# Kernel optimization log

Hardware: AMD Instinct MI355X
Metric: run time of the kernel (lower is better)

Reference implementation:

```python
import jax, jax.numpy as jnp
import numpy as np

B, T, H, S, A, E = 256, 64, 2048, 512, 64, 2048


def setup_inputs() -> dict:
    key = jax.random.key(0)
    ks = jax.random.split(key, 16)
    def w(k, shape, fan_in):
        return (jax.random.normal(k, shape, dtype=jnp.float32) / np.float32(np.sqrt(fan_in)))
    return {
        "prev_hidden": jax.random.normal(ks[0], (B, H), dtype=jnp.float32),
        "prev_state": jax.random.normal(ks[1], (B, S), dtype=jnp.float32),
        "actions": jax.random.normal(ks[2], (B, T, A), dtype=jnp.float32),
        "obs": jax.random.normal(ks[3], (B, T, E), dtype=jnp.float32),
        "prior_noise": jax.random.normal(ks[4], (B, T - 1, S), dtype=jnp.float32),
        "post_noise": jax.random.normal(ks[5], (B, T - 1, S), dtype=jnp.float32),
        # project_state_action: Linear(A+S -> H), stored [in, out]
        "W_sa": w(ks[6], (S + A, H), S + A), "b_sa": jnp.zeros((H,), jnp.float32),
        # GRUCell weights in torch layout [3H, in]
        "W_ih": w(ks[7], (3 * H, H), H), "W_hh": w(ks[8], (3 * H, H), H),
        "b_ih": jnp.zeros((3 * H,), jnp.float32), "b_hh": jnp.zeros((3 * H,), jnp.float32),
        # project_hidden_action: Linear(H+A -> H)
        "W_ha": w(ks[9], (H + A, H), H + A), "b_ha": jnp.zeros((H,), jnp.float32),
        # prior: Linear(H -> 2S)
        "W_prior": w(ks[10], (H, 2 * S), H), "b_prior": jnp.zeros((2 * S,), jnp.float32),
        # project_hidden_obs: Linear(H+E -> H)
        "W_ho": w(ks[11], (H + E, H), H + E), "b_ho": jnp.zeros((H,), jnp.float32),
        # posterior: Linear(H -> 2S)
        "W_post": w(ks[12], (H, 2 * S), H), "b_post": jnp.zeros((2 * S,), jnp.float32),
        "stop": 0,
    }


def reference(prev_hidden, prev_state, actions, obs, prior_noise, post_noise,
              W_sa, b_sa, W_ih, W_hh, b_ih, b_hh, W_ha, b_ha,
              W_prior, b_prior, W_ho, b_ho, W_post, b_post, stop):
    relu = jax.nn.relu

    def gru(x, h):
        gi = x @ W_ih.T + b_ih  # [B, 3H]
        gh = h @ W_hh.T + b_hh
        ir, iz, inn = jnp.split(gi, 3, axis=-1)
        hr, hz, hn = jnp.split(gh, 3, axis=-1)
        r = jax.nn.sigmoid(ir + hr)
        z = jax.nn.sigmoid(iz + hz)
        n = jnp.tanh(inn + r * hn)
        return (1.0 - z) * n + z * h

    def step(carry, xs):
        h, s = carry  # h: [B,H] hidden, s: [B,S] posterior state (obs is given)
        a, o, pn, qn = xs
        sa = relu(jnp.concatenate([s, a], axis=-1) @ W_sa + b_sa)
        h = gru(sa, h)
        ha = relu(jnp.concatenate([h, a], axis=-1) @ W_ha + b_ha)
        pm, plv = jnp.split(ha @ W_prior + b_prior, 2, axis=-1)
        ps = pm + jnp.exp(jax.nn.softplus(plv)) * pn  # prior rsample
        ho = relu(jnp.concatenate([h, o], axis=-1) @ W_ho + b_ho)
        qm, qlv = jnp.split(ho @ W_post + b_post, 2, axis=-1)
        qs = qm + jnp.exp(jax.nn.softplus(qlv)) * qn  # posterior rsample
        return (h, qs), (h, ps, qs, pm, plv, qm, qlv)

    Tm1 = actions.shape[1] - 1
    xs = (jnp.swapaxes(actions[:, :Tm1], 0, 1),
          jnp.swapaxes(obs[:, :Tm1], 0, 1),
          jnp.swapaxes(prior_noise, 0, 1),
          jnp.swapaxes(post_noise, 0, 1))
    _, ys = jax.lax.scan(step, (prev_hidden, prev_state), xs)
    hs, ps, qs, pm, plv, qm, qlv = (jnp.swapaxes(y, 0, 1) for y in ys)
    hiddens = jnp.concatenate([prev_hidden[:, None, :], hs], axis=1)       # [B, T, H]
    prior_states = jnp.concatenate([prev_state[:, None, :], ps], axis=1)   # [B, T, S]
    posterior_states = jnp.concatenate([prev_state[:, None, :], qs], axis=1)
    return (hiddens, prior_states, posterior_states, pm, plv, qm, qlv)
```

## Files before the change

kernel.cpp:

```cpp
#include <hip/hip_runtime.h>


typedef __attribute__((ext_vector_type(8))) short bf16x8;
typedef __attribute__((ext_vector_type(4))) float f32x4;
typedef __attribute__((ext_vector_type(4))) short s16x4;

#define DEVI static __device__ __forceinline__

DEVI float bf2f(short s) { union { float f; unsigned u; } v; v.u = ((unsigned)(unsigned short)s) << 16; return v.f; }
DEVI short f2bf(float f) {
  union { float f; unsigned u; } v; v.f = f;
  unsigned r = v.u + 0x7FFFu + ((v.u >> 16) & 1u);
  return (short)(r >> 16);
}

#define Bsz 256
#define Tsz 64
#define Hsz 2048
#define Ssz 512
#define Asz 64
#define Esz 2048
#define TM1 63

#define PSH (256 * 2048)
#define PSS (256 * 1024)

#define OUT_PS  33554432L
#define OUT_QS  41943040L
#define OUT_PM  50331648L
#define OUT_PLV 58589184L
#define OUT_QM  66846720L
#define OUT_QLV 75104256L

struct GArg {
  const short* A; const short* Bt; const float* bias; const short* Ci;
  float* oF; short* oB;
  int lda, ldb, ldoF, ldoB; long ldci, pstride;
};

template<int HASBIAS, int HASCI, int RELU, int OUTF, int OUTB>
__global__ __launch_bounds__(256) void gemm_bt(GArg g0, GArg g1, int kcK) {
  const int gemm = blockIdx.z & 1, kc = blockIdx.z >> 1;
  const GArg g = gemm ? g1 : g0;
  const short* __restrict__ Ag = g.A + (long)kc * kcK;
  const short* __restrict__ Bg = g.Bt + (long)kc * kcK;
  __shared__ __align__(16) short As[2][128 * 64];
  __shared__ __align__(16) short Bs[2][128 * 64];
  const int tid = threadIdx.x;
  const int w = tid >> 6, l = tid & 63;
  const int bm0 = blockIdx.y << 7, bn0 = blockIdx.x << 7;
  const int fc = l & 15, fh = l >> 4;
  const int wr = (w >> 1) << 6, wc = (w & 1) << 6;
  const int rx = fc & 7;

  const int srccol = ((l & 7) ^ ((l >> 3) & 7)) << 3;
  long aoff[4], boff[4];
#pragma unroll
  for (int i = 0; i < 4; ++i) {
    const int row = (((i << 2) + w) << 3) + (l >> 3);
    aoff[i] = (long)(bm0 + row) * g.lda + srccol;
    boff[i] = (long)(bn0 + row) * g.ldb + srccol;
  }

  f32x4 acc[4][4];
#pragma unroll
  for (int i = 0; i < 4; ++i)
#pragma unroll
    for (int j = 0; j < 4; ++j) acc[i][j] = f32x4{0.f, 0.f, 0.f, 0.f};

  auto STAGE = [&](int kt, int buf) {
#pragma unroll
    for (int i = 0; i < 4; ++i) {
      const int ib = ((i << 2) + w) << 10;
      __builtin_amdgcn_global_load_lds(
          (const __attribute__((address_space(1))) void*)(Ag + aoff[i] + (kt << 6)),
          (__attribute__((address_space(3))) void*)((char*)&As[buf][0] + ib), 16, 0, 0);
      __builtin_amdgcn_global_load_lds(
          (const __attribute__((address_space(1))) void*)(Bg + boff[i] + (kt << 6)),
          (__attribute__((address_space(3))) void*)((char*)&Bs[buf][0] + ib), 16, 0, 0);
    }
  };
  auto COMPUTE = [&](int buf) {
#pragma unroll
    for (int kk = 0; kk < 2; ++kk) {
      bf16x8 af[4], bb[4];
#pragma unroll
      for (int mi = 0; mi < 4; ++mi)
        af[mi] = *(const bf16x8*)&As[buf][(wr + (mi << 4) + fc) * 64 + ((((kk << 2) + fh) ^ rx) << 3)];
#pragma unroll
      for (int ni = 0; ni < 4; ++ni)
        bb[ni] = *(const bf16x8*)&Bs[buf][(wc + (ni << 4) + fc) * 64 + ((((kk << 2) + fh) ^ rx) << 3)];
#pragma unroll
      for (int mi = 0; mi < 4; ++mi)
#pragma unroll
        for (int ni = 0; ni < 4; ++ni)
          acc[mi][ni] = __builtin_amdgcn_mfma_f32_16x16x32_bf16(af[mi], bb[ni], acc[mi][ni], 0, 0, 0);
    }
  };

  const int nk = kcK >> 6;
  STAGE(0, 0);
  for (int kt = 0; kt < nk - 1; ++kt) {
    STAGE(kt + 1, (kt + 1) & 1);
    asm volatile("s_waitcnt vmcnt(8)" ::: "memory");
    __builtin_amdgcn_s_barrier();
    __builtin_amdgcn_sched_barrier(0);
    COMPUTE(kt & 1);
    asm volatile("s_waitcnt lgkmcnt(0)" ::: "memory");
    __builtin_amdgcn_s_barrier();
  }
  asm volatile("s_waitcnt vmcnt(0)" ::: "memory");
  __builtin_amdgcn_s_barrier();
  __builtin_amdgcn_sched_barrier(0);
  COMPUTE((nk - 1) & 1);

  float* oF = OUTF ? (g.oF + (long)kc * g.pstride) : (float*)nullptr;
#pragma unroll
  for (int mi = 0; mi < 4; ++mi) {
#pragma unroll
    for (int ni = 0; ni < 4; ++ni) {
      const int n = bn0 + wc + (ni << 4) + fc;
      float bv = 0.f;
      if (HASBIAS) bv = g.bias[n];
#pragma unroll
      for (int r = 0; r < 4; ++r) {
        const int m = bm0 + wr + (mi << 4) + (fh << 2) + r;
        float v = acc[mi][ni][r] + bv;
        if (HASCI) v += bf2f(g.Ci[(long)m * g.ldci + n]);
        if (RELU) v = fmaxf(v, 0.f);
        if (OUTF) oF[(long)m * g.ldoF + n] = v;
        if (OUTB) g.oB[(long)m * g.ldoB + n] = f2bf(v);
      }
    }
  }
}

__global__ void conv_f2b(const float* __restrict__ src, short* __restrict__ dst, long n) {
  long i = ((long)blockIdx.x * 256 + threadIdx.x) * 4;
  const long stride = (long)gridDim.x * 1024;
  for (; i < n; i += stride) {
    float4 v = *(const float4*)(src + i);
    s16x4 o;
    o[0] = f2bf(v.x); o[1] = f2bf(v.y); o[2] = f2bf(v.z); o[3] = f2bf(v.w);
    *(s16x4*)(dst + i) = o;
  }
}

__global__ void transp(const float* __restrict__ src, short* __restrict__ dst,
                       int srcld, int k0, int K, int N) {
  __shared__ float t[32][33];
  const int tx = threadIdx.x, ty = threadIdx.y;
  const int kb = blockIdx.y << 5, nb = blockIdx.x << 5;
#pragma unroll
  for (int i = ty; i < 32; i += 8)
    t[i][tx] = src[(long)(k0 + kb + i) * srcld + nb + tx];
  __syncthreads();
#pragma unroll
  for (int i = ty; i < 32; i += 8)
    dst[(long)(nb + i) * K + kb + tx] = f2bf(t[tx][i]);
}

__global__ void init_kernel(const float* __restrict__ ph, const float* __restrict__ ps,
                            float* __restrict__ out, short* __restrict__ hb, short* __restrict__ sb) {
  const int idx = blockIdx.x * 256 + threadIdx.x;
  const int b = idx >> 11, n = idx & 2047;
  const float h = ph[idx];
  out[(long)b * (Tsz * Hsz) + n] = h;
  hb[idx] = f2bf(h);
  if (n < Ssz) {
    const int sidx = b * Ssz + n;
    const float s = ps[sidx];
    out[OUT_PS + (long)b * (Tsz * Ssz) + n] = s;
    out[OUT_QS + (long)b * (Tsz * Ssz) + n] = s;
    sb[sidx] = f2bf(s);
  }
}

__global__ void gru_kernel(const float* __restrict__ gi, const float* __restrict__ gh,
                           const float* __restrict__ b_ih, const float* __restrict__ b_hh,
                           const float* __restrict__ hold, float* __restrict__ hnew,
                           short* __restrict__ hb) {
  const int idx = blockIdx.x * 256 + threadIdx.x;
  const int b = idx >> 11, n = idx & 2047;
  const long gb = (long)b * (3 * Hsz) + n;
  const float ir = gi[gb] + b_ih[n],                 hr = gh[gb] + b_hh[n];
  const float iz = gi[gb + Hsz] + b_ih[Hsz + n],     hz = gh[gb + Hsz] + b_hh[Hsz + n];
  const float in_ = gi[gb + 2 * Hsz] + b_ih[2 * Hsz + n];
  const float hn = gh[gb + 2 * Hsz] + b_hh[2 * Hsz + n];
  const float r = 1.f / (1.f + expf(-(ir + hr)));
  const float z = 1.f / (1.f + expf(-(iz + hz)));
  const float nn = tanhf(in_ + r * hn);
  const float h = (1.f - z) * nn + z * hold[(long)b * (Tsz * Hsz) + n];
  hnew[(long)b * (Tsz * Hsz) + n] = h;
  hb[idx] = f2bf(h);
}

__global__ void reduce_relu4(const float* __restrict__ p, const short* __restrict__ ciA,
                             const short* __restrict__ ciB, short* __restrict__ oA,
                             short* __restrict__ oB, int t) {
  const int z = blockIdx.y;
  const float* pz = p + (long)z * 4 * PSH;
  const short* ci = z ? ciB : ciA;
  short* o = z ? oB : oA;
  const int i = (blockIdx.x * 256 + threadIdx.x) * 4;
  const int b = i >> 11, n = i & 2047;
  f32x4 v = *(const f32x4*)&pz[i];
  v += *(const f32x4*)&pz[PSH + i];
  v += *(const f32x4*)&pz[2 * PSH + i];
  v += *(const f32x4*)&pz[3 * PSH + i];
  const s16x4 c = *(const s16x4*)&ci[((long)b * Tsz + t) * Hsz + n];
  s16x4 ov;
#pragma unroll
  for (int k = 0; k < 4; ++k) ov[k] = f2bf(fmaxf(v[k] + bf2f(c[k]), 0.f));
  *(s16x4*)&o[i] = ov;
}

__global__ void sample_kernel(const float* __restrict__ pp,
                              const float* __restrict__ bp, const float* __restrict__ bq,
                              const float* __restrict__ pn, const float* __restrict__ qn,
                              float* __restrict__ out, short* __restrict__ sb, int t) {
  const int idx = blockIdx.x * 256 + threadIdx.x;
  const int b = idx >> 9, j = idx & 511;
  const float* pr = pp;
  const float* po = pp + 4L * PSS;
  const long r0 = (long)b * 1024 + j;
  float pm = bp[j], plv = bp[512 + j], qm = bq[j], qlv = bq[512 + j];
#pragma unroll
  for (int k = 0; k < 4; ++k) {
    pm  += pr[k * PSS + r0];  plv += pr[k * PSS + r0 + 512];
    qm  += po[k * PSS + r0];  qlv += po[k * PSS + r0 + 512];
  }
  const long noff = ((long)b * TM1 + t) * Ssz + j;
  const float psv = pm + (1.f + expf(plv)) * pn[noff];
  const float qsv = qm + (1.f + expf(qlv)) * qn[noff];
  out[OUT_PS + (long)b * (Tsz * Ssz) + (long)(t + 1) * Ssz + j] = psv;
  out[OUT_QS + (long)b * (Tsz * Ssz) + (long)(t + 1) * Ssz + j] = qsv;
  out[OUT_PM  + noff] = pm;
  out[OUT_PLV + noff] = plv;
  out[OUT_QM  + noff] = qm;
  out[OUT_QLV + noff] = qlv;
  sb[idx] = f2bf(qsv);
}

static GArg mk(const short* A, int lda, const short* Bt, int ldb, const float* bias,
               const short* Ci, long ldci, float* oF, int ldoF, long pstride,
               short* oB, int ldoB) {
  GArg g; g.A = A; g.Bt = Bt; g.bias = bias; g.Ci = Ci; g.ldci = ldci;
  g.oF = oF; g.oB = oB; g.lda = lda; g.ldb = ldb; g.ldoF = ldoF; g.ldoB = ldoB;
  g.pstride = pstride;
  return g;
}

extern "C" void kernel_launch(void* const* d_in, const int* in_sizes, int n_in,
                              void* d_out, int out_size, void* d_ws, size_t ws_size,
                              hipStream_t stream) {
  const float* prev_hidden = (const float*)d_in[0];
  const float* prev_state  = (const float*)d_in[1];
  const float* actions     = (const float*)d_in[2];
  const float* obs         = (const float*)d_in[3];
  const float* prior_noise = (const float*)d_in[4];
  const float* post_noise  = (const float*)d_in[5];
  const float* W_sa = (const float*)d_in[6];
  const float* b_sa = (const float*)d_in[7];
  const float* W_ih = (const float*)d_in[8];
  const float* W_hh = (const float*)d_in[9];
  const float* b_ih = (const float*)d_in[10];
  const float* b_hh = (const float*)d_in[11];
  const float* W_ha = (const float*)d_in[12];
  const float* b_ha = (const float*)d_in[13];
  const float* W_prior = (const float*)d_in[14];
  const float* b_prior = (const float*)d_in[15];
  const float* W_ho = (const float*)d_in[16];
  const float* b_ho = (const float*)d_in[17];
  const float* W_post = (const float*)d_in[18];
  const float* b_post = (const float*)d_in[19];
  float* out = (float*)d_out;

  char* p = (char*)d_ws;
  auto alloc = [&](size_t bytes) { char* r = p; p += (bytes + 255) & ~(size_t)255; return r; };
  short* Wih_b   = (short*)alloc(3L * Hsz * Hsz * 2);
  short* Whh_b   = (short*)alloc(3L * Hsz * Hsz * 2);
  short* Wt_sa_s = (short*)alloc((long)Hsz * Ssz * 2);
  short* Wt_sa_a = (short*)alloc((long)Hsz * Asz * 2);
  short* Wt_ha_h = (short*)alloc((long)Hsz * Hsz * 2);
  short* Wt_ha_a = (short*)alloc((long)Hsz * Asz * 2);
  short* Wt_ho_h = (short*)alloc((long)Hsz * Hsz * 2);
  short* Wt_ho_o = (short*)alloc((long)Hsz * Esz * 2);
  short* Wt_pr   = (short*)alloc(2L * Ssz * Hsz * 2);
  short* Wt_po   = (short*)alloc(2L * Ssz * Hsz * 2);
  short* obs_b   = (short*)alloc((long)Bsz * Tsz * Esz * 2);
  short* act_b   = (short*)alloc((long)Bsz * Tsz * Asz * 2);
  short* a_pre   = (short*)alloc((long)Bsz * Tsz * Hsz * 2);
  short* ha_a    = (short*)alloc((long)Bsz * Tsz * Hsz * 2);
  short* ho_o    = (short*)alloc((long)Bsz * Tsz * Hsz * 2);
  short* s_b     = (short*)alloc((long)Bsz * Ssz * 2);
  short* h_b     = (short*)alloc((long)Bsz * Hsz * 2);
  short* sa_b    = (short*)alloc((long)Bsz * Hsz * 2);
  short* ha_b    = (short*)alloc((long)Bsz * Hsz * 2);
  short* ho_b    = (short*)alloc((long)Bsz * Hsz * 2);
  char* q = (char*)obs_b;
  auto alias = [&](size_t bytes) { char* r = q; q += (bytes + 255) & ~(size_t)255; return r; };
  float* gi_f    = (float*)alias((long)Bsz * 3 * Hsz * 4);
  float* gh_f    = (float*)alias((long)Bsz * 3 * Hsz * 4);
  float* haho_p  = (float*)alias(8L * PSH * 4);
  float* prpo_p  = (float*)alias(8L * PSS * 4);
  (void)ws_size; (void)in_sizes; (void)n_in; (void)out_size;

  conv_f2b<<<4096, 256, 0, stream>>>(obs,  obs_b, (long)Bsz * Tsz * Esz);
  conv_f2b<<<1024, 256, 0, stream>>>(actions, act_b, (long)Bsz * Tsz * Asz);
  conv_f2b<<<4096, 256, 0, stream>>>(W_ih, Wih_b, 3L * Hsz * Hsz);
  conv_f2b<<<4096, 256, 0, stream>>>(W_hh, Whh_b, 3L * Hsz * Hsz);

  dim3 tb(32, 8);
  transp<<<dim3(Hsz / 32, Ssz / 32), tb, 0, stream>>>(W_sa, Wt_sa_s, Hsz, 0,   Ssz, Hsz);
  transp<<<dim3(Hsz / 32, Asz / 32), tb, 0, stream>>>(W_sa, Wt_sa_a, Hsz, Ssz, Asz, Hsz);
  transp<<<dim3(Hsz / 32, Hsz / 32), tb, 0, stream>>>(W_ha, Wt_ha_h, Hsz, 0,   Hsz, Hsz);
  transp<<<dim3(Hsz / 32, Asz / 32), tb, 0, stream>>>(W_ha, Wt_ha_a, Hsz, Hsz, Asz, Hsz);
  transp<<<dim3(Hsz / 32, Hsz / 32), tb, 0, stream>>>(W_ho, Wt_ho_h, Hsz, 0,   Hsz, Hsz);
  transp<<<dim3(Hsz / 32, Esz / 32), tb, 0, stream>>>(W_ho, Wt_ho_o, Hsz, Hsz, Esz, Hsz);
  transp<<<dim3(2 * Ssz / 32, Hsz / 32), tb, 0, stream>>>(W_prior, Wt_pr, 2 * Ssz, 0, Hsz, 2 * Ssz);
  transp<<<dim3(2 * Ssz / 32, Hsz / 32), tb, 0, stream>>>(W_post,  Wt_po, 2 * Ssz, 0, Hsz, 2 * Ssz);

  init_kernel<<<2048, 256, 0, stream>>>(prev_hidden, prev_state, out, h_b, s_b);

  {
    GArg g0 = mk(act_b, Asz, Wt_sa_a, Asz, b_sa, nullptr, 0, nullptr, 0, 0, a_pre, Hsz);
    GArg g1 = mk(act_b, Asz, Wt_ha_a, Asz, b_ha, nullptr, 0, nullptr, 0, 0, ha_a, Hsz);
    gemm_bt<1, 0, 0, 0, 1><<<dim3(Hsz / 128, (Bsz * Tsz) / 128, 2), 256, 0, stream>>>(g0, g1, Asz);
  }
  {
    GArg g0 = mk(obs_b, Esz, Wt_ho_o, Esz, b_ho, nullptr, 0, nullptr, 0, 0, ho_o, Hsz);
    gemm_bt<1, 0, 0, 0, 1><<<dim3(Hsz / 128, (Bsz * Tsz) / 128, 1), 256, 0, stream>>>(g0, g0, Esz);
  }

  const long ldPre = (long)Tsz * Hsz;
  for (int t = 0; t < TM1; ++t) {
    {
      GArg g0 = mk(s_b, Ssz, Wt_sa_s, Ssz, nullptr, a_pre + (long)t * Hsz, ldPre,
                   nullptr, 0, 0, sa_b, Hsz);
      gemm_bt<0, 1, 1, 0, 1><<<dim3(16, 2, 1), 256, 0, stream>>>(g0, g0, Ssz);
    }
    {
      GArg g0 = mk(sa_b, Hsz, Wih_b, Hsz, nullptr, nullptr, 0, gi_f, 3 * Hsz, 0, nullptr, 0);
      GArg g1 = mk(h_b,  Hsz, Whh_b, Hsz, nullptr, nullptr, 0, gh_f, 3 * Hsz, 0, nullptr, 0);
      gemm_bt<0, 0, 0, 1, 0><<<dim3(48, 2, 2), 256, 0, stream>>>(g0, g1, Hsz);
    }
    gru_kernel<<<2048, 256, 0, stream>>>(gi_f, gh_f, b_ih, b_hh,
                                         out + (long)t * Hsz, out + (long)(t + 1) * Hsz, h_b);
    {
      GArg g0 = mk(h_b, Hsz, Wt_ha_h, Hsz, nullptr, nullptr, 0, haho_p, Hsz, PSH, nullptr, 0);
      GArg g1 = mk(h_b, Hsz, Wt_ho_h, Hsz, nullptr, nullptr, 0, haho_p + 4L * PSH, Hsz, PSH, nullptr, 0);
      gemm_bt<0, 0, 0, 1, 0><<<dim3(16, 2, 8), 256, 0, stream>>>(g0, g1, Hsz / 4);
    }
    reduce_relu4<<<dim3(512, 2), 256, 0, stream>>>(haho_p, ha_a, ho_o, ha_b, ho_b, t);
    {
      GArg g0 = mk(ha_b, Hsz, Wt_pr, Hsz, nullptr, nullptr, 0, prpo_p, 2 * Ssz, PSS, nullptr, 0);
      GArg g1 = mk(ho_b, Hsz, Wt_po, Hsz, nullptr, nullptr, 0, prpo_p + 4L * PSS, 2 * Ssz, PSS, nullptr, 0);
      gemm_bt<0, 0, 0, 1, 0><<<dim3(8, 2, 8), 256, 0, stream>>>(g0, g1, Hsz / 4);
    }
    sample_kernel<<<512, 256, 0, stream>>>(prpo_p, b_prior, b_post,
                                           prior_noise, post_noise, out, s_b, t);
  }
}
```

Measured before the change: 6.638 ms.

## Hoist prior branch out of recurrence into batched GEMMs and fuse sampling epilogue

The prior path (ha projection, prior head, prior sampling) does not feed the recurrence, so it is removed from the per-step loop. The bf16 hidden states are stored for every step, and the prior path then runs once over all B*T rows as two large GEMMs. The posterior head GEMM gets a fused sampling epilogue: the prior/posterior weights are row-permuted so mean and logvar columns land in the same tile, which replaces the split-K partials and the separate sample kernel. This cuts per-step launches and work on the serial critical path, at the cost of an extra Bsz*T*H bf16 buffer and a posterior GEMM that now runs without split-K over only 16 blocks.

After: 8.211 ms. 1.24x slower.

```diff
diff --git a/kernel.cpp b/kernel.cpp
--- a/kernel.cpp
+++ b/kernel.cpp
@@ -23,7 +23,6 @@
 #define TM1 63
 
 #define PSH (256 * 2048)
-#define PSS (256 * 1024)
 
 #define OUT_PS  33554432L
 #define OUT_QS  41943040L
@@ -39,8 +38,10 @@
 };
 
 template<int HASBIAS, int HASCI, int RELU, int OUTF, int OUTB>
-__global__ __launch_bounds__(256) void gemm_bt(GArg g0, GArg g1, int kcK) {
-  const int gemm = blockIdx.z & 1, kc = blockIdx.z >> 1;
+__global__ __launch_bounds__(256) void gemm_bt(GArg g0, GArg g1, int glog, int kcK) {
+  const int z = blockIdx.z;
+  const int gemm = glog ? (z & 1) : 0;
+  const int kc = z >> glog;
   const GArg g = gemm ? g1 : g0;
   const short* __restrict__ Ag = g.A + (long)kc * kcK;
   const short* __restrict__ Bg = g.Bt + (long)kc * kcK;
@@ -135,6 +136,108 @@
   }
 }
 
+template<int PERSTEP>
+__global__ __launch_bounds__(256) void gemm_sample(
+    const short* __restrict__ A, const short* __restrict__ Bt,
+    const float* __restrict__ bias, const float* __restrict__ noise,
+    float* __restrict__ out, short* __restrict__ sbOut,
+    long outS, long outM, long outLV, int t_arg) {
+  __shared__ __align__(16) short As[2][128 * 64];
+  __shared__ __align__(16) short Bs[2][128 * 64];
+  const int tid = threadIdx.x;
+  const int w = tid >> 6, l = tid & 63;
+  const int bm0 = blockIdx.y << 7, bn0 = blockIdx.x << 7;
+  const int fc = l & 15, fh = l >> 4;
+  const int wr = (w >> 1) << 6, wc = (w & 1) << 6;
+  const int rx = fc & 7;
+
+  const int srccol = ((l & 7) ^ ((l >> 3) & 7)) << 3;
+  long aoff[4], boff[4];
+#pragma unroll
+  for (int i = 0; i < 4; ++i) {
+    const int row = (((i << 2) + w) << 3) + (l >> 3);
+    aoff[i] = (long)(bm0 + row) * Hsz + srccol;
+    boff[i] = (long)(bn0 + row) * Hsz + srccol;
+  }
+
+  f32x4 acc[4][4];
+#pragma unroll
+  for (int i = 0; i < 4; ++i)
+#pragma unroll
+    for (int j = 0; j < 4; ++j) acc[i][j] = f32x4{0.f, 0.f, 0.f, 0.f};
+
+  auto STAGE = [&](int kt, int buf) {
+#pragma unroll
+    for (int i = 0; i < 4; ++i) {
+      const int ib = ((i << 2) + w) << 10;
+      __builtin_amdgcn_global_load_lds(
+          (const __attribute__((address_space(1))) void*)(A + aoff[i] + (kt << 6)),
+          (__attribute__((address_space(3))) void*)((char*)&As[buf][0] + ib), 16, 0, 0);
+      __builtin_amdgcn_global_load_lds(
+          (const __attribute__((address_space(1))) void*)(Bt + boff[i] + (kt << 6)),
+          (__attribute__((address_space(3))) void*)((char*)&Bs[buf][0] + ib), 16, 0, 0);
+    }
+  };
+  auto COMPUTE = [&](int buf) {
+#pragma unroll
+    for (int kk = 0; kk < 2; ++kk) {
+      bf16x8 af[4], bb[4];
+#pragma unroll
+      for (int mi = 0; mi < 4; ++mi)
+        af[mi] = *(const bf16x8*)&As[buf][(wr + (mi << 4) + fc) * 64 + ((((kk << 2) + fh) ^ rx) << 3)];
+#pragma unroll
+      for (int ni = 0; ni < 4; ++ni)
+        bb[ni] = *(const bf16x8*)&Bs[buf][(wc + (ni << 4) + fc) * 64 + ((((kk << 2) + fh) ^ rx) << 3)];
+#pragma unroll
+      for (int mi = 0; mi < 4; ++mi)
+#pragma unroll
+        for (int ni = 0; ni < 4; ++ni)
+          acc[mi][ni] = __builtin_amdgcn_mfma_f32_16x16x32_bf16(af[mi], bb[ni], acc[mi][ni], 0, 0, 0);
+    }
+  };
+
+  const int nk = Hsz >> 6;
+  STAGE(0, 0);
+  for (int kt = 0; kt < nk - 1; ++kt) {
+    STAGE(kt + 1, (kt + 1) & 1);
+    asm volatile("s_waitcnt vmcnt(8)" ::: "memory");
+    __builtin_amdgcn_s_barrier();
+    __builtin_amdgcn_sched_barrier(0);
+    COMPUTE(kt & 1);
+    asm volatile("s_waitcnt lgkmcnt(0)" ::: "memory");
+    __builtin_amdgcn_s_barrier();
+  }
+  asm volatile("s_waitcnt vmcnt(0)" ::: "memory");
+  __builtin_amdgcn_s_barrier();
+  __builtin_amdgcn_sched_barrier(0);
+  COMPUTE((nk - 1) & 1);
+
+#pragma unroll
+  for (int mi = 0; mi < 4; ++mi) {
+#pragma unroll
+    for (int nh = 0; nh < 2; ++nh) {
+      const int ni = nh << 1;
+      const int j = (((bn0 + wc + (ni << 4)) >> 5) << 4) + fc;
+      const float bm = bias[j], blv = bias[512 + j];
+#pragma unroll
+      for (int r = 0; r < 4; ++r) {
+        const int m = bm0 + wr + (mi << 4) + (fh << 2) + r;
+        int b, t;
+        if (PERSTEP) { b = m; t = t_arg; }
+        else { b = m >> 6; t = m & 63; if (t == TM1) continue; }
+        const float mv = acc[mi][ni][r] + bm;
+        const float lv = acc[mi][ni + 1][r] + blv;
+        const long noff = ((long)b * TM1 + t) * Ssz + j;
+        const float sv = mv + (1.f + expf(lv)) * noise[noff];
+        out[outS + (long)b * (Tsz * Ssz) + (long)(t + 1) * Ssz + j] = sv;
+        out[outM + noff] = mv;
+        out[outLV + noff] = lv;
+        if (PERSTEP) sbOut[b * Ssz + j] = f2bf(sv);
+      }
+    }
+  }
+}
+
 __global__ void conv_f2b(const float* __restrict__ src, short* __restrict__ dst, long n) {
   long i = ((long)blockIdx.x * 256 + threadIdx.x) * 4;
   const long stride = (long)gridDim.x * 1024;
@@ -146,6 +249,7 @@
   }
 }
 
+template<int PERM>
 __global__ void transp(const float* __restrict__ src, short* __restrict__ dst,
                        int srcld, int k0, int K, int N) {
   __shared__ float t[32][33];
@@ -156,8 +260,11 @@
     t[i][tx] = src[(long)(k0 + kb + i) * srcld + nb + tx];
   __syncthreads();
 #pragma unroll
-  for (int i = ty; i < 32; i += 8)
-    dst[(long)(nb + i) * K + kb + tx] = f2bf(t[tx][i]);
+  for (int i = ty; i < 32; i += 8) {
+    int n = nb + i, drow = n;
+    if (PERM) { const int j = n & 511, lv = n >> 9; drow = ((j >> 4) << 5) | (lv << 4) | (j & 15); }
+    dst[(long)drow * K + kb + tx] = f2bf(t[tx][i]);
+  }
 }
 
 __global__ void init_kernel(const float* __restrict__ ph, const float* __restrict__ ps,
@@ -179,7 +286,7 @@
 __global__ void gru_kernel(const float* __restrict__ gi, const float* __restrict__ gh,
                            const float* __restrict__ b_ih, const float* __restrict__ b_hh,
                            const float* __restrict__ hold, float* __restrict__ hnew,
-                           short* __restrict__ hb) {
+                           short* __restrict__ hb, short* __restrict__ hallRow) {
   const int idx = blockIdx.x * 256 + threadIdx.x;
   const int b = idx >> 11, n = idx & 2047;
   const long gb = (long)b * (3 * Hsz) + n;
@@ -192,54 +299,24 @@
   const float nn = tanhf(in_ + r * hn);
   const float h = (1.f - z) * nn + z * hold[(long)b * (Tsz * Hsz) + n];
   hnew[(long)b * (Tsz * Hsz) + n] = h;
-  hb[idx] = f2bf(h);
-}
-
-__global__ void reduce_relu4(const float* __restrict__ p, const short* __restrict__ ciA,
-                             const short* __restrict__ ciB, short* __restrict__ oA,
-                             short* __restrict__ oB, int t) {
-  const int z = blockIdx.y;
-  const float* pz = p + (long)z * 4 * PSH;
-  const short* ci = z ? ciB : ciA;
-  short* o = z ? oB : oA;
+  const short hbf = f2bf(h);
+  hb[idx] = hbf;
+  hallRow[(long)b * (Tsz * Hsz) + n] = hbf;
+}
+
+__global__ void reduce_relu(const float* __restrict__ p, const short* __restrict__ ci,
+                            short* __restrict__ o, int t) {
   const int i = (blockIdx.x * 256 + threadIdx.x) * 4;
   const int b = i >> 11, n = i & 2047;
-  f32x4 v = *(const f32x4*)&pz[i];
-  v += *(const f32x4*)&pz[PSH + i];
-  v += *(const f32x4*)&pz[2 * PSH + i];
-  v += *(const f32x4*)&pz[3 * PSH + i];
+  f32x4 v = *(const f32x4*)&p[i];
+  v += *(const f32x4*)&p[PSH + i];
+  v += *(const f32x4*)&p[2 * PSH + i];
+  v += *(const f32x4*)&p[3 * PSH + i];
   const s16x4 c = *(const s16x4*)&ci[((long)b * Tsz + t) * Hsz + n];
   s16x4 ov;
 #pragma unroll
   for (int k = 0; k < 4; ++k) ov[k] = f2bf(fmaxf(v[k] + bf2f(c[k]), 0.f));
   *(s16x4*)&o[i] = ov;
-}
-
-__global__ void sample_kernel(const float* __restrict__ pp,
-                              const float* __restrict__ bp, const float* __restrict__ bq,
-                              const float* __restrict__ pn, const float* __restrict__ qn,
-                              float* __restrict__ out, short* __restrict__ sb, int t) {
-  const int idx = blockIdx.x * 256 + threadIdx.x;
-  const int b = idx >> 9, j = idx & 511;
-  const float* pr = pp;
-  const float* po = pp + 4L * PSS;
-  const long r0 = (long)b * 1024 + j;
-  float pm = bp[j], plv = bp[512 + j], qm = bq[j], qlv = bq[512 + j];
-#pragma unroll
-  for (int k = 0; k < 4; ++k) {
-    pm  += pr[k * PSS + r0];  plv += pr[k * PSS + r0 + 512];
-    qm  += po[k * PSS + r0];  qlv += po[k * PSS + r0 + 512];
-  }
-  const long noff = ((long)b * TM1 + t) * Ssz + j;
-  const float psv = pm + (1.f + expf(plv)) * pn[noff];
-  const float qsv = qm + (1.f + expf(qlv)) * qn[noff];
-  out[OUT_PS + (long)b * (Tsz * Ssz) + (long)(t + 1) * Ssz + j] = psv;
-  out[OUT_QS + (long)b * (Tsz * Ssz) + (long)(t + 1) * Ssz + j] = qsv;
-  out[OUT_PM  + noff] = pm;
-  out[OUT_PLV + noff] = plv;
-  out[OUT_QM  + noff] = qm;
-  out[OUT_QLV + noff] = qlv;
-  sb[idx] = f2bf(qsv);
 }
 
 static GArg mk(const short* A, int lda, const short* Bt, int ldb, const float* bias,
@@ -293,17 +370,16 @@
   short* a_pre   = (short*)alloc((long)Bsz * Tsz * Hsz * 2);
   short* ha_a    = (short*)alloc((long)Bsz * Tsz * Hsz * 2);
   short* ho_o    = (short*)alloc((long)Bsz * Tsz * Hsz * 2);
+  short* Hall_b  = (short*)alloc((long)Bsz * Tsz * Hsz * 2);
   short* s_b     = (short*)alloc((long)Bsz * Ssz * 2);
   short* h_b     = (short*)alloc((long)Bsz * Hsz * 2);
   short* sa_b    = (short*)alloc((long)Bsz * Hsz * 2);
-  short* ha_b    = (short*)alloc((long)Bsz * Hsz * 2);
   short* ho_b    = (short*)alloc((long)Bsz * Hsz * 2);
   char* q = (char*)obs_b;
   auto alias = [&](size_t bytes) { char* r = q; q += (bytes + 255) & ~(size_t)255; return r; };
   float* gi_f    = (float*)alias((long)Bsz * 3 * Hsz * 4);
   float* gh_f    = (float*)alias((long)Bsz * 3 * Hsz * 4);
-  float* haho_p  = (float*)alias(8L * PSH * 4);
-  float* prpo_p  = (float*)alias(8L * PSS * 4);
+  float* ho_p    = (float*)alias(4L * PSH * 4);
   (void)ws_size; (void)in_sizes; (void)n_in; (void)out_size;
 
   conv_f2b<<<4096, 256, 0, stream>>>(obs,  obs_b, (long)Bsz * Tsz * Esz);
@@ -312,25 +388,25 @@
   conv_f2b<<<4096, 256, 0, stream>>>(W_hh, Whh_b, 3L * Hsz * Hsz);
 
   dim3 tb(32, 8);
-  transp<<<dim3(Hsz / 32, Ssz / 32), tb, 0, stream>>>(W_sa, Wt_sa_s, Hsz, 0,   Ssz, Hsz);
-  transp<<<dim3(Hsz / 32, Asz / 32), tb, 0, stream>>>(W_sa, Wt_sa_a, Hsz, Ssz, Asz, Hsz);
-  transp<<<dim3(Hsz / 32, Hsz / 32), tb, 0, stream>>>(W_ha, Wt_ha_h, Hsz, 0,   Hsz, Hsz);
-  transp<<<dim3(Hsz / 32, Asz / 32), tb, 0, stream>>>(W_ha, Wt_ha_a, Hsz, Hsz, Asz, Hsz);
-  transp<<<dim3(Hsz / 32, Hsz / 32), tb, 0, stream>>>(W_ho, Wt_ho_h, Hsz, 0,   Hsz, Hsz);
-  transp<<<dim3(Hsz / 32, Esz / 32), tb, 0, stream>>>(W_ho, Wt_ho_o, Hsz, Hsz, Esz, Hsz);
-  transp<<<dim3(2 * Ssz / 32, Hsz / 32), tb, 0, stream>>>(W_prior, Wt_pr, 2 * Ssz, 0, Hsz, 2 * Ssz);
-  transp<<<dim3(2 * Ssz / 32, Hsz / 32), tb, 0, stream>>>(W_post,  Wt_po, 2 * Ssz, 0, Hsz, 2 * Ssz);
+  transp<0><<<dim3(Hsz / 32, Ssz / 32), tb, 0, stream>>>(W_sa, Wt_sa_s, Hsz, 0,   Ssz, Hsz);
+  transp<0><<<dim3(Hsz / 32, Asz / 32), tb, 0, stream>>>(W_sa, Wt_sa_a, Hsz, Ssz, Asz, Hsz);
+  transp<0><<<dim3(Hsz / 32, Hsz / 32), tb, 0, stream>>>(W_ha, Wt_ha_h, Hsz, 0,   Hsz, Hsz);
+  transp<0><<<dim3(Hsz / 32, Asz / 32), tb, 0, stream>>>(W_ha, Wt_ha_a, Hsz, Hsz, Asz, Hsz);
+  transp<0><<<dim3(Hsz / 32, Hsz / 32), tb, 0, stream>>>(W_ho, Wt_ho_h, Hsz, 0,   Hsz, Hsz);
+  transp<0><<<dim3(Hsz / 32, Esz / 32), tb, 0, stream>>>(W_ho, Wt_ho_o, Hsz, Hsz, Esz, Hsz);
+  transp<1><<<dim3(2 * Ssz / 32, Hsz / 32), tb, 0, stream>>>(W_prior, Wt_pr, 2 * Ssz, 0, Hsz, 2 * Ssz);
+  transp<1><<<dim3(2 * Ssz / 32, Hsz / 32), tb, 0, stream>>>(W_post,  Wt_po, 2 * Ssz, 0, Hsz, 2 * Ssz);
 
   init_kernel<<<2048, 256, 0, stream>>>(prev_hidden, prev_state, out, h_b, s_b);
 
   {
     GArg g0 = mk(act_b, Asz, Wt_sa_a, Asz, b_sa, nullptr, 0, nullptr, 0, 0, a_pre, Hsz);
     GArg g1 = mk(act_b, Asz, Wt_ha_a, Asz, b_ha, nullptr, 0, nullptr, 0, 0, ha_a, Hsz);
-    gemm_bt<1, 0, 0, 0, 1><<<dim3(Hsz / 128, (Bsz * Tsz) / 128, 2), 256, 0, stream>>>(g0, g1, Asz);
+    gemm_bt<1, 0, 0, 0, 1><<<dim3(Hsz / 128, (Bsz * Tsz) / 128, 2), 256, 0, stream>>>(g0, g1, 1, Asz);
   }
   {
     GArg g0 = mk(obs_b, Esz, Wt_ho_o, Esz, b_ho, nullptr, 0, nullptr, 0, 0, ho_o, Hsz);
-    gemm_bt<1, 0, 0, 0, 1><<<dim3(Hsz / 128, (Bsz * Tsz) / 128, 1), 256, 0, stream>>>(g0, g0, Esz);
+    gemm_bt<1, 0, 0, 0, 1><<<dim3(Hsz / 128, (Bsz * Tsz) / 128, 1), 256, 0, stream>>>(g0, g0, 0, Esz);
   }
 
   const long ldPre = (long)Tsz * Hsz;
@@ -338,27 +414,29 @@
     {
       GArg g0 = mk(s_b, Ssz, Wt_sa_s, Ssz, nullptr, a_pre + (long)t * Hsz, ldPre,
                    nullptr, 0, 0, sa_b, Hsz);
-      gemm_bt<0, 1, 1, 0, 1><<<dim3(16, 2, 1), 256, 0, stream>>>(g0, g0, Ssz);
+      gemm_bt<0, 1, 1, 0, 1><<<dim3(16, 2, 1), 256, 0, stream>>>(g0, g0, 0, Ssz);
     }
     {
       GArg g0 = mk(sa_b, Hsz, Wih_b, Hsz, nullptr, nullptr, 0, gi_f, 3 * Hsz, 0, nullptr, 0);
       GArg g1 = mk(h_b,  Hsz, Whh_b, Hsz, nullptr, nullptr, 0, gh_f, 3 * Hsz, 0, nullptr, 0);
-      gemm_bt<0, 0, 0, 1, 0><<<dim3(48, 2, 2), 256, 0, stream>>>(g0, g1, Hsz);
+      gemm_bt<0, 0, 0, 1, 0><<<dim3(48, 2, 2), 256, 0, stream>>>(g0, g1, 1, Hsz);
     }
     gru_kernel<<<2048, 256, 0, stream>>>(gi_f, gh_f, b_ih, b_hh,
-                                         out + (long)t * Hsz, out + (long)(t + 1) * Hsz, h_b);
+                                         out + (long)t * Hsz, out + (long)(t + 1) * Hsz,
+                                         h_b, Hall_b + (long)t * Hsz);
     {
-      GArg g0 = mk(h_b, Hsz, Wt_ha_h, Hsz, nullptr, nullptr, 0, haho_p, Hsz, PSH, nullptr, 0);
-      GArg g1 = mk(h_b, Hsz, Wt_ho_h, Hsz, nullptr, nullptr, 0, haho_p + 4L * PSH, Hsz, PSH, nullptr, 0);
-      gemm_bt<0, 0, 0, 1, 0><<<dim3(16, 2, 8), 256, 0, stream>>>(g0, g1, Hsz / 4);
-    }
-    reduce_relu4<<<dim3(512, 2), 256, 0, stream>>>(haho_p, ha_a, ho_o, ha_b, ho_b, t);
-    {
-      GArg g0 = mk(ha_b, Hsz, Wt_pr, Hsz, nullptr, nullptr, 0, prpo_p, 2 * Ssz, PSS, nullptr, 0);
-      GArg g1 = mk(ho_b, Hsz, Wt_po, Hsz, nullptr, nullptr, 0, prpo_p + 4L * PSS, 2 * Ssz, PSS, nullptr, 0);
-      gemm_bt<0, 0, 0, 1, 0><<<dim3(8, 2, 8), 256, 0, stream>>>(g0, g1, Hsz / 4);
-    }
-    sample_kernel<<<512, 256, 0, stream>>>(prpo_p, b_prior, b_post,
-                                           prior_noise, post_noise, out, s_b, t);
-  }
-}
+      GArg g0 = mk(h_b, Hsz, Wt_ho_h, Hsz, nullptr, nullptr, 0, ho_p, Hsz, PSH, nullptr, 0);
+      gemm_bt<0, 0, 0, 1, 0><<<dim3(16, 2, 4), 256, 0, stream>>>(g0, g0, 0, Hsz / 4);
+    }
+    reduce_relu<<<512, 256, 0, stream>>>(ho_p, ho_o, ho_b, t);
+    gemm_sample<1><<<dim3(8, 2, 1), 256, 0, stream>>>(
+        ho_b, Wt_po, b_post, post_noise, out, s_b, OUT_QS, OUT_QM, OUT_QLV, t);
+  }
+
+  {
+    GArg g0 = mk(Hall_b, Hsz, Wt_ha_h, Hsz, nullptr, ha_a, Hsz, nullptr, 0, 0, a_pre, Hsz);
+    gemm_bt<0, 1, 1, 0, 1><<<dim3(16, 128, 1), 256, 0, stream>>>(g0, g0, 0, Hsz);
+  }
+  gemm_sample<0><<<dim3(8, 128, 1), 256, 0, stream>>>(
+      a_pre, Wt_pr, b_prior, prior_noise, out, nullptr, OUT_PS, OUT_PM, OUT_PLV, 0);
+}
```

## Fuse GRU gate GEMMs with elementwise GRU update via permuted weights

Applied to the files above, without the earlier changes.

Replaces the separate gi/gh GEMM plus gru_kernel with one kernel. It computes both input and hidden projections per tile and applies the GRU nonlinearity in the epilogue. Weights are reordered at setup so each 48-column group holds the r/z/n rows for 16 hidden units, and the hidden bf16 buffer is double-buffered so reads and writes of h do not race. This removes the fp32 gi/gh round trip through global memory and one launch per step. In exchange the tiles are smaller (64x96) with more LDS per block, which may lower occupancy or MFMA efficiency.

Result: no change. 6.572 ms (-1.0%).

```diff
diff --git a/kernel.cpp b/kernel.cpp
--- a/kernel.cpp
+++ b/kernel.cpp
@@ -44,8 +44,8 @@
   const GArg g = gemm ? g1 : g0;
   const short* __restrict__ Ag = g.A + (long)kc * kcK;
   const short* __restrict__ Bg = g.Bt + (long)kc * kcK;
-  __shared__ __align__(16) short As[2][128 * 64];
-  __shared__ __align__(16) short Bs[2][128 * 64];
+  __shared__ __align__(16) short As[2][8192];
+  __shared__ __align__(16) short Bs[2][8192];
   const int tid = threadIdx.x;
   const int w = tid >> 6, l = tid & 63;
   const int bm0 = blockIdx.y << 7, bn0 = blockIdx.x << 7;
@@ -135,6 +135,129 @@
   }
 }
 
+__global__ __launch_bounds__(256) void gigh_gru(
+    const short* __restrict__ sa, const short* __restrict__ hb_in,
+    const short* __restrict__ Wih, const short* __restrict__ Whh,
+    const float* __restrict__ b_ih, const float* __restrict__ b_hh,
+    const float* __restrict__ hold, float* __restrict__ hnew,
+    short* __restrict__ hb_out) {
+  __shared__ __align__(16) short AsS[2][4096];
+  __shared__ __align__(16) short AsH[2][4096];
+  __shared__ __align__(16) short BsI[2][6144];
+  __shared__ __align__(16) short BsH[2][6144];
+  const int tid = threadIdx.x;
+  const int w = tid >> 6, l = tid & 63;
+  const int bm0 = blockIdx.y << 6;
+  const int bn0 = blockIdx.x * 96;
+  const int fc = l & 15, fh = l >> 4;
+  const int wr = (w >> 1) << 5;
+  const int wn = (w & 1) * 48;
+  const int rx = fc & 7;
+  const int srccol = ((l & 7) ^ ((l >> 3) & 7)) << 3;
+
+  long aoff[2], boff[3];
+#pragma unroll
+  for (int i = 0; i < 2; ++i) {
+    const int row = (((i << 2) + w) << 3) + (l >> 3);
+    aoff[i] = (long)(bm0 + row) * Hsz + srccol;
+  }
+#pragma unroll
+  for (int i = 0; i < 3; ++i) {
+    const int row = (((i << 2) + w) << 3) + (l >> 3);
+    boff[i] = (long)(bn0 + row) * Hsz + srccol;
+  }
+
+  f32x4 acc_i[2][3], acc_h[2][3];
+#pragma unroll
+  for (int i = 0; i < 2; ++i)
+#pragma unroll
+    for (int j = 0; j < 3; ++j) { acc_i[i][j] = f32x4{0.f,0.f,0.f,0.f}; acc_h[i][j] = f32x4{0.f,0.f,0.f,0.f}; }
+
+  auto STAGE = [&](int kt, int buf) {
+#pragma unroll
+    for (int i = 0; i < 2; ++i) {
+      const int ib = ((i << 2) + w) << 10;
+      __builtin_amdgcn_global_load_lds(
+          (const __attribute__((address_space(1))) void*)(sa + aoff[i] + (kt << 6)),
+          (__attribute__((address_space(3))) void*)((char*)&AsS[0][0] + (buf << 13) + ib), 16, 0, 0);
+      __builtin_amdgcn_global_load_lds(
+          (const __attribute__((address_space(1))) void*)(hb_in + aoff[i] + (kt << 6)),
+          (__attribute__((address_space(3))) void*)((char*)&AsH[0][0] + (buf << 13) + ib), 16, 0, 0);
+    }
+#pragma unroll
+    for (int i = 0; i < 3; ++i) {
+      const int ib = ((i << 2) + w) << 10;
+      __builtin_amdgcn_global_load_lds(
+          (const __attribute__((address_space(1))) void*)(Wih + boff[i] + (kt << 6)),
+          (__attribute__((address_space(3))) void*)((char*)&BsI[0][0] + buf * 12288 + ib), 16, 0, 0);
+      __builtin_amdgcn_global_load_lds(
+          (const __attribute__((address_space(1))) void*)(Whh + boff[i] + (kt << 6)),
+          (__attribute__((address_space(3))) void*)((char*)&BsH[0][0] + buf * 12288 + ib), 16, 0, 0);
+    }
+  };
+  auto COMPUTE = [&](int buf) {
+#pragma unroll
+    for (int kk = 0; kk < 2; ++kk) {
+      const int sw = (((kk << 2) + fh) ^ rx) << 3;
+      bf16x8 as_[2], ah_[2], bi_[3], bh_[3];
+#pragma unroll
+      for (int mi = 0; mi < 2; ++mi) {
+        as_[mi] = *(const bf16x8*)&AsS[buf][(wr + (mi << 4) + fc) * 64 + sw];
+        ah_[mi] = *(const bf16x8*)&AsH[buf][(wr + (mi << 4) + fc) * 64 + sw];
+      }
+#pragma unroll
+      for (int ni = 0; ni < 3; ++ni) {
+        bi_[ni] = *(const bf16x8*)&BsI[buf][(wn + (ni << 4) + fc) * 64 + sw];
+        bh_[ni] = *(const bf16x8*)&BsH[buf][(wn + (ni << 4) + fc) * 64 + sw];
+      }
+#pragma unroll
+      for (int mi = 0; mi < 2; ++mi)
+#pragma unroll
+        for (int ni = 0; ni < 3; ++ni) {
+          acc_i[mi][ni] = __builtin_amdgcn_mfma_f32_16x16x32_bf16(as_[mi], bi_[ni], acc_i[mi][ni], 0, 0, 0);
+          acc_h[mi][ni] = __builtin_amdgcn_mfma_f32_16x16x32_bf16(ah_[mi], bh_[ni], acc_h[mi][ni], 0, 0, 0);
+        }
+    }
+  };
+
+  const int nk = Hsz >> 6;
+  STAGE(0, 0);
+  for (int kt = 0; kt < nk - 1; ++kt) {
+    STAGE(kt + 1, (kt + 1) & 1);
+    asm volatile("s_waitcnt vmcnt(10)" ::: "memory");
+    __builtin_amdgcn_s_barrier();
+    __builtin_amdgcn_sched_barrier(0);
+    COMPUTE(kt & 1);
+    asm volatile("s_waitcnt lgkmcnt(0)" ::: "memory");
+    __builtin_amdgcn_s_barrier();
+  }
+  asm volatile("s_waitcnt vmcnt(0)" ::: "memory");
+  __builtin_amdgcn_s_barrier();
+  __builtin_amdgcn_sched_barrier(0);
+  COMPUTE((nk - 1) & 1);
+
+  const int j = (((int)blockIdx.x << 1) + (w & 1)) * 16 + fc;
+  const float bir = b_ih[j],            bhr = b_hh[j];
+  const float biz = b_ih[Hsz + j],      bhz = b_hh[Hsz + j];
+  const float bin = b_ih[2 * Hsz + j],  bhn = b_hh[2 * Hsz + j];
+#pragma unroll
+  for (int mi = 0; mi < 2; ++mi) {
+#pragma unroll
+    for (int r = 0; r < 4; ++r) {
+      const int m = bm0 + wr + (mi << 4) + (fh << 2) + r;
+      const float ir = acc_i[mi][0][r] + bir, hr = acc_h[mi][0][r] + bhr;
+      const float iz = acc_i[mi][1][r] + biz, hz = acc_h[mi][1][r] + bhz;
+      const float in_ = acc_i[mi][2][r] + bin, hn = acc_h[mi][2][r] + bhn;
+      const float rg = 1.f / (1.f + expf(-(ir + hr)));
+      const float zg = 1.f / (1.f + expf(-(iz + hz)));
+      const float ng = tanhf(in_ + rg * hn);
+      const float hv = (1.f - zg) * ng + zg * hold[(long)m * (Tsz * Hsz) + j];
+      hnew[(long)m * (Tsz * Hsz) + j] = hv;
+      hb_out[m * Hsz + j] = f2bf(hv);
+    }
+  }
+}
+
 __global__ void conv_f2b(const float* __restrict__ src, short* __restrict__ dst, long n) {
   long i = ((long)blockIdx.x * 256 + threadIdx.x) * 4;
   const long stride = (long)gridDim.x * 1024;
@@ -144,6 +267,18 @@
     o[0] = f2bf(v.x); o[1] = f2bf(v.y); o[2] = f2bf(v.z); o[3] = f2bf(v.w);
     *(s16x4*)(dst + i) = o;
   }
+}
+
+__global__ void conv_perm48(const float* __restrict__ src, short* __restrict__ dst) {
+  const long e = ((long)blockIdx.x * 256 + threadIdx.x) * 4;
+  const int np = (int)(e >> 11), col = (int)(e & 2047);
+  const int u = np / 48, rem = np - u * 48;
+  const int g = rem >> 4, jlo = rem & 15;
+  const long srow = ((long)g << 11) + u * 16 + jlo;
+  float4 v = *(const float4*)&src[srow * 2048 + col];
+  s16x4 o;
+  o[0] = f2bf(v.x); o[1] = f2bf(v.y); o[2] = f2bf(v.z); o[3] = f2bf(v.w);
+  *(s16x4*)&dst[e] = o;
 }
 
 __global__ void transp(const float* __restrict__ src, short* __restrict__ dst,
@@ -174,25 +309,6 @@
     out[OUT_QS + (long)b * (Tsz * Ssz) + n] = s;
     sb[sidx] = f2bf(s);
   }
-}
-
-__global__ void gru_kernel(const float* __restrict__ gi, const float* __restrict__ gh,
-                           const float* __restrict__ b_ih, const float* __restrict__ b_hh,
-                           const float* __restrict__ hold, float* __restrict__ hnew,
-                           short* __restrict__ hb) {
-  const int idx = blockIdx.x * 256 + threadIdx.x;
-  const int b = idx >> 11, n = idx & 2047;
-  const long gb = (long)b * (3 * Hsz) + n;
-  const float ir = gi[gb] + b_ih[n],                 hr = gh[gb] + b_hh[n];
-  const float iz = gi[gb + Hsz] + b_ih[Hsz + n],     hz = gh[gb + Hsz] + b_hh[Hsz + n];
-  const float in_ = gi[gb + 2 * Hsz] + b_ih[2 * Hsz + n];
-  const float hn = gh[gb + 2 * Hsz] + b_hh[2 * Hsz + n];
-  const float r = 1.f / (1.f + expf(-(ir + hr)));
-  const float z = 1.f / (1.f + expf(-(iz + hz)));
-  const float nn = tanhf(in_ + r * hn);
-  const float h = (1.f - z) * nn + z * hold[(long)b * (Tsz * Hsz) + n];
-  hnew[(long)b * (Tsz * Hsz) + n] = h;
-  hb[idx] = f2bf(h);
 }
 
 __global__ void reduce_relu4(const float* __restrict__ p, const short* __restrict__ ciA,
@@ -278,8 +394,8 @@
 
   char* p = (char*)d_ws;
   auto alloc = [&](size_t bytes) { char* r = p; p += (bytes + 255) & ~(size_t)255; return r; };
-  short* Wih_b   = (short*)alloc(3L * Hsz * Hsz * 2);
-  short* Whh_b   = (short*)alloc(3L * Hsz * Hsz * 2);
+  short* Wih_p   = (short*)alloc(3L * Hsz * Hsz * 2);
+  short* Whh_p   = (short*)alloc(3L * Hsz * Hsz * 2);
   short* Wt_sa_s = (short*)alloc((long)Hsz * Ssz * 2);
   short* Wt_sa_a = (short*)alloc((long)Hsz * Asz * 2);
   short* Wt_ha_h = (short*)alloc((long)Hsz * Hsz * 2);
@@ -294,22 +410,21 @@
   short* ha_a    = (short*)alloc((long)Bsz * Tsz * Hsz * 2);
   short* ho_o    = (short*)alloc((long)Bsz * Tsz * Hsz * 2);
   short* s_b     = (short*)alloc((long)Bsz * Ssz * 2);
-  short* h_b     = (short*)alloc((long)Bsz * Hsz * 2);
+  short* h_b1    = (short*)alloc((long)Bsz * Hsz * 2);
+  short* h_b2    = (short*)alloc((long)Bsz * Hsz * 2);
   short* sa_b    = (short*)alloc((long)Bsz * Hsz * 2);
   short* ha_b    = (short*)alloc((long)Bsz * Hsz * 2);
   short* ho_b    = (short*)alloc((long)Bsz * Hsz * 2);
   char* q = (char*)obs_b;
   auto alias = [&](size_t bytes) { char* r = q; q += (bytes + 255) & ~(size_t)255; return r; };
-  float* gi_f    = (float*)alias((long)Bsz * 3 * Hsz * 4);
-  float* gh_f    = (float*)alias((long)Bsz * 3 * Hsz * 4);
   float* haho_p  = (float*)alias(8L * PSH * 4);
   float* prpo_p  = (float*)alias(8L * PSS * 4);
   (void)ws_size; (void)in_sizes; (void)n_in; (void)out_size;
 
   conv_f2b<<<4096, 256, 0, stream>>>(obs,  obs_b, (long)Bsz * Tsz * Esz);
   conv_f2b<<<1024, 256, 0, stream>>>(actions, act_b, (long)Bsz * Tsz * Asz);
-  conv_f2b<<<4096, 256, 0, stream>>>(W_ih, Wih_b, 3L * Hsz * Hsz);
-  conv_f2b<<<4096, 256, 0, stream>>>(W_hh, Whh_b, 3L * Hsz * Hsz);
+  conv_perm48<<<12288, 256, 0, stream>>>(W_ih, Wih_p);
+  conv_perm48<<<12288, 256, 0, stream>>>(W_hh, Whh_p);
 
   dim3 tb(32, 8);
   transp<<<dim3(Hsz / 32, Ssz / 32), tb, 0, stream>>>(W_sa, Wt_sa_s, Hsz, 0,   Ssz, Hsz);
@@ -321,7 +436,7 @@
   transp<<<dim3(2 * Ssz / 32, Hsz / 32), tb, 0, stream>>>(W_prior, Wt_pr, 2 * Ssz, 0, Hsz, 2 * Ssz);
   transp<<<dim3(2 * Ssz / 32, Hsz / 32), tb, 0, stream>>>(W_post,  Wt_po, 2 * Ssz, 0, Hsz, 2 * Ssz);
 
-  init_kernel<<<2048, 256, 0, stream>>>(prev_hidden, prev_state, out, h_b, s_b);
+  init_kernel<<<2048, 256, 0, stream>>>(prev_hidden, prev_state, out, h_b1, s_b);
 
   {
     GArg g0 = mk(act_b, Asz, Wt_sa_a, Asz, b_sa, nullptr, 0, nullptr, 0, 0, a_pre, Hsz);
@@ -335,21 +450,19 @@
 
   const long ldPre = (long)Tsz * Hsz;
   for (int t = 0; t < TM1; ++t) {
+    short* hp = (t & 1) ? h_b2 : h_b1;
+    short* hn = (t & 1) ? h_b1 : h_b2;
     {
       GArg g0 = mk(s_b, Ssz, Wt_sa_s, Ssz, nullptr, a_pre + (long)t * Hsz, ldPre,
                    nullptr, 0, 0, sa_b, Hsz);
       gemm_bt<0, 1, 1, 0, 1><<<dim3(16, 2, 1), 256, 0, stream>>>(g0, g0, Ssz);
     }
+    gigh_gru<<<dim3(64, 4, 1), 256, 0, stream>>>(
+        sa_b, hp, Wih_p, Whh_p, b_ih, b_hh,
+        out + (long)t * Hsz, out + (long)(t + 1) * Hsz, hn);
     {
-      GArg g0 = mk(sa_b, Hsz, Wih_b, Hsz, nullptr, nullptr, 0, gi_f, 3 * Hsz, 0, nullptr, 0);
-      GArg g1 = mk(h_b,  Hsz, Whh_b, Hsz, nullptr, nullptr, 0, gh_f, 3 * Hsz, 0, nullptr, 0);
-      gemm_bt<0, 0, 0, 1, 0><<<dim3(48, 2, 2), 256, 0, stream>>>(g0, g1, Hsz);
-    }
-    gru_kernel<<<2048, 256, 0, stream>>>(gi_f, gh_f, b_ih, b_hh,
-                                         out + (long)t * Hsz, out + (long)(t + 1) * Hsz, h_b);
-    {
-      GArg g0 = mk(h_b, Hsz, Wt_ha_h, Hsz, nullptr, nullptr, 0, haho_p, Hsz, PSH, nullptr, 0);
-      GArg g1 = mk(h_b, Hsz, Wt_ho_h, Hsz, nullptr, nullptr, 0, haho_p + 4L * PSH, Hsz, PSH, nullptr, 0);
+      GArg g0 = mk(hn, Hsz, Wt_ha_h, Hsz, nullptr, nullptr, 0, haho_p, Hsz, PSH, nullptr, 0);
+      GArg g1 = mk(hn, Hsz, Wt_ho_h, Hsz, nullptr, nullptr, 0, haho_p + 4L * PSH, Hsz, PSH, nullptr, 0);
       gemm_bt<0, 0, 0, 1, 0><<<dim3(16, 2, 8), 256, 0, stream>>>(g0, g1, Hsz / 4);
     }
     reduce_relu4<<<dim3(512, 2), 256, 0, stream>>>(haho_p, ha_a, ho_o, ha_b, ho_b, t);
```
